# Optimization experiments

Measured on AMD Instinct MI355X. Metric: run time of the kernel, lower is better.

Reference implementation:

```python
import jax, jax.numpy as jnp
import numpy as np
import jax.scipy.linalg

BATCH = 1048576
M_NUM = 2
DT = 0.0166667
NN_RATIO = 0.5
SLOPE = 0.01  # torch LeakyReLU default negative_slope


def setup_inputs() -> dict:
    key = jax.random.key(0)
    ks = jax.random.split(key, 16)
    inp = {}
    inp["SS"] = jax.random.normal(ks[0], (BATCH, 2), dtype=jnp.float32)
    inp["Alphas"] = jax.random.uniform(ks[1], (BATCH, M_NUM), dtype=jnp.float32)
    # per-muscle scalar parameters (positive so sqrt(K*I) is valid)
    inp["K0s"] = jax.random.uniform(ks[2], (M_NUM,), minval=0.5, maxval=1.5)
    inp["K1s"] = jax.random.uniform(ks[3], (M_NUM,), minval=0.5, maxval=1.5)
    inp["L0s"] = jax.random.uniform(ks[4], (M_NUM,), minval=0.5, maxval=1.5)
    inp["L1s"] = jax.random.uniform(ks[5], (M_NUM,), minval=0.1, maxval=0.6)
    inp["Ms"] = jnp.array([1.0, -1.0], dtype=jnp.float32)  # moment arms
    inp["I_p"] = jnp.array([1.0], dtype=jnp.float32)
    inp["B_p"] = jnp.array([0.05], dtype=jnp.float32)
    inp["K_p"] = jnp.array([1.0], dtype=jnp.float32)
    # per-muscle compensational MLP weights: 3-32-32-32-1 (eval mode, dropout off)
    s = 0.1
    inp["W1"] = jax.random.normal(ks[6], (M_NUM, 3, 32)) * s
    inp["b1"] = jax.random.normal(ks[7], (M_NUM, 32)) * s
    inp["W2"] = jax.random.normal(ks[8], (M_NUM, 32, 32)) * s
    inp["b2"] = jax.random.normal(ks[9], (M_NUM, 32)) * s
    inp["W3"] = jax.random.normal(ks[10], (M_NUM, 32, 32)) * s
    inp["b3"] = jax.random.normal(ks[11], (M_NUM, 32)) * s
    inp["W4"] = jax.random.normal(ks[12], (M_NUM, 32, 1)) * s
    inp["b4"] = jax.random.normal(ks[13], (M_NUM, 1)) * s
    return inp


def _leaky(x):
    return jnp.where(x >= 0, x, SLOPE * x)


def reference(SS, Alphas, K0s, K1s, L0s, L1s, Ms, I_p, B_p, K_p,
              W1, b1, W2, b2, W3, b3, W4, b4):
    B = SS.shape[0]
    a = jnp.clip(Alphas, 0.0, 1.0)                      # (B, m)
    # muscle length / speed via scalar moment arms
    l = SS[:, 0:1] * Ms[None, :]                        # (B, m)
    dl = SS[:, 1:2] * Ms[None, :]                       # (B, m)
    # compensational MLPs, vectorized over muscles
    x = jnp.stack([l, dl, a], axis=-1)                  # (B, m, 3)
    h = _leaky(jnp.einsum('bmi,mio->bmo', x, W1) + b1[None])
    h = _leaky(jnp.einsum('bmi,mio->bmo', h, W2) + b2[None])
    h = _leaky(jnp.einsum('bmi,mio->bmo', h, W3) + b3[None])
    nn_out = jnp.tanh(jnp.einsum('bmi,mio->bmo', h, W4) + b4[None])[..., 0] * NN_RATIO  # (B, m)

    I0, B0p, K0p = I_p[0], B_p[0], K_p[0]
    K_m = K0s[None, :] + K1s[None, :] * a               # (B, m)
    K_tot = jnp.sum(K_m * Ms[None, :] ** 2, axis=1)     # (B,)
    A10 = -(K_tot + K0p) / I0
    D = 2.0 * jnp.sqrt(K_tot * I0)
    A11 = -(D + B0p) / I0
    B_F = K_m * (L0s[None, :] + L1s[None, :] * a - jnp.abs(l)) \
        + K1s[None, :] * L1s[None, :] * a * a * nn_out   # (B, m)
    B10 = jnp.sum(B_F * Ms[None, :], axis=1) / I0       # (B,)

    # Build block matrix M6 = [[A*dt, B*dt, 0], [0, 0, I2], [0, 0, 0]]
    M6 = jnp.zeros((B, 6, 6), dtype=SS.dtype)
    M6 = M6.at[:, 0, 1].set(DT)
    M6 = M6.at[:, 1, 0].set(A10 * DT)
    M6 = M6.at[:, 1, 1].set(A11 * DT)
    M6 = M6.at[:, 1, 2].set(B10 * DT)
    M6 = M6.at[:, 1, 3].set(DT / I0)
    M6 = M6.at[:, 2, 4].set(1.0)
    M6 = M6.at[:, 3, 5].set(1.0)

    expMT = jax.vmap(jax.scipy.linalg.expm)(M6)         # (B, 6, 6)
    Ad = expMT[:, :2, :2]
    Bd1 = expMT[:, :2, 4:6]
    Bd0 = expMT[:, :2, 2:4] - Bd1
    u = jnp.array([1.0, 0.0], dtype=SS.dtype)           # U0 = U1 = [1, 0]
    SSout = (jnp.einsum('bij,bj->bi', Ad, SS)
             + jnp.einsum('bij,j->bi', Bd0, u)
             + jnp.einsum('bij,j->bi', Bd1, u))          # (B, 2)
    return SSout[:, :1], SSout
```

## Files before the change

### kernel.cpp

```cpp
#include <hip/hip_runtime.h>
#include <hip/hip_bf16.h>

#define NTHREADS 256
#define WAVES    4
#define GPW      4
#define DT_F     0.0166667f

typedef _Float16 f16x4 __attribute__((ext_vector_type(4)));
typedef _Float16 f16x2 __attribute__((ext_vector_type(2)));
typedef __fp16   hf2   __attribute__((ext_vector_type(2)));
typedef float    f32x4 __attribute__((ext_vector_type(4)));

#define BF16_PROBE 0xBF803F80u

#define OW1 0
#define OB1 192
#define OW2 256
#define OB2 2304
#define OW3 2368
#define OB3 4416
#define OW4 4480
#define OB4 4544
#define SMEM_F 4560

__device__ __forceinline__ float leaky(float x) { return fmaxf(x, 0.01f * x); }

__device__ __forceinline__ float tanh_fast(float x) {
    const float xc = fminf(fmaxf(x, -10.0f), 10.0f);
    const float t  = __expf(2.0f * xc);
    return (t - 1.0f) * __builtin_amdgcn_rcpf(t + 1.0f);
}

__device__ __forceinline__ f16x2 pkrtz(float a, float b) {
    return __builtin_bit_cast(f16x2, __builtin_amdgcn_cvt_pkrtz(a, b));
}

__device__ __forceinline__ f16x4 leaky_cvt(const f32x4 D) {
    f16x2 lo = pkrtz(D[0], D[1]);
    f16x2 hi = pkrtz(D[2], D[3]);
    const f16x2 sl = {(_Float16)0.01f, (_Float16)0.01f};
    lo = __builtin_elementwise_max(lo, lo * sl);
    hi = __builtin_elementwise_max(hi, hi * sl);
    return __builtin_shufflevector(lo, hi, 0, 1, 2, 3);
}

__device__ __forceinline__ void epilogue_math(
    const float* P, float ss0, float ss1, float a0, float a1,
    float nn0, float nn1, float& o0f, float& o1f)
{
    const float K00 = P[0], K01 = P[1], K10 = P[2], K11 = P[3];
    const float L00 = P[4], L01 = P[5], L10 = P[6], L11 = P[7];
    const float Ms0 = P[8], Ms1 = P[9];
    const float I0  = P[10], B0p = P[11], K0p = P[12];

    const float Km0   = fmaf(K10, a0, K00);
    const float Km1   = fmaf(K11, a1, K01);
    const float K_tot = Km0*Ms0*Ms0 + Km1*Ms1*Ms1;
    const float invI  = 1.0f / I0;
    const float A10   = -(K_tot + K0p) * invI;
    const float Dd    = 2.0f * sqrtf(K_tot * I0);
    const float A11   = -(Dd + B0p) * invI;
    const float absl0 = fabsf(ss0 * Ms0);
    const float absl1 = fabsf(ss0 * Ms1);
    const float BF0   = Km0 * (L00 + L10*a0 - absl0) + K10*L10*a0*a0*nn0;
    const float BF1   = Km1 * (L01 + L11*a1 - absl1) + K11*L11*a1*a1*nn1;
    const float B10   = (BF0*Ms0 + BF1*Ms1) * invI;

    const float t01 = DT_F;
    const float t10 = A10 * DT_F;
    const float t11 = A11 * DT_F;

    float p00 = 1.0f/5040.0f, p01 = 0.0f, p10 = 0.0f, p11 = 1.0f/5040.0f;
    const float coef[6] = {1.0f/720.0f, 1.0f/120.0f, 1.0f/24.0f,
                           1.0f/6.0f,   0.5f,        1.0f};
    #pragma unroll
    for (int j = 0; j < 6; ++j) {
        const float cj  = coef[j];
        const float n00 = p01*t10 + cj;
        const float n01 = p00*t01 + p01*t11;
        const float n10 = p11*t10;
        const float n11 = p10*t01 + p11*t11 + cj;
        p00 = n00; p01 = n01; p10 = n10; p11 = n11;
    }
    const float e00 = 1.0f + t01*p10;
    const float e01 = t01*p11;
    const float e10 = t10*p00 + t11*p10;
    const float e11 = 1.0f + t10*p01 + t11*p11;

    const float cscale = DT_F * B10;
    o0f = fmaf(e00, ss0, fmaf(e01, ss1, p01 * cscale));
    o1f = fmaf(e10, ss0, fmaf(e11, ss1, p11 * cscale));
}

__device__ __forceinline__ float ldb(const __hip_bfloat16* p, int i) {
    return __bfloat162float(p[i]);
}

__device__ void run_bf16_fallback(
    const void* SSv, const void* ALv, const void* K0sv, const void* K1sv,
    const void* L0sv, const void* L1sv, const void* Msv, const void* I_pv,
    const void* B_pv, const void* K_pv, const void* W1v, const void* b1v,
    const void* W2v, const void* b2v, const void* W3v, const void* b3v,
    const void* W4v, const void* b4v, void* outv, int batch)
{
    const __hip_bfloat16* SS = (const __hip_bfloat16*)SSv;
    const __hip_bfloat16* AL = (const __hip_bfloat16*)ALv;
    const __hip_bfloat16* W1 = (const __hip_bfloat16*)W1v;
    const __hip_bfloat16* b1 = (const __hip_bfloat16*)b1v;
    const __hip_bfloat16* W2 = (const __hip_bfloat16*)W2v;
    const __hip_bfloat16* b2 = (const __hip_bfloat16*)b2v;
    const __hip_bfloat16* W3 = (const __hip_bfloat16*)W3v;
    const __hip_bfloat16* b3 = (const __hip_bfloat16*)b3v;
    const __hip_bfloat16* W4 = (const __hip_bfloat16*)W4v;
    const __hip_bfloat16* b4 = (const __hip_bfloat16*)b4v;

    float P[13];
    P[0] = ldb((const __hip_bfloat16*)K0sv, 0); P[1] = ldb((const __hip_bfloat16*)K0sv, 1);
    P[2] = ldb((const __hip_bfloat16*)K1sv, 0); P[3] = ldb((const __hip_bfloat16*)K1sv, 1);
    P[4] = ldb((const __hip_bfloat16*)L0sv, 0); P[5] = ldb((const __hip_bfloat16*)L0sv, 1);
    P[6] = ldb((const __hip_bfloat16*)L1sv, 0); P[7] = ldb((const __hip_bfloat16*)L1sv, 1);
    P[8] = ldb((const __hip_bfloat16*)Msv, 0);  P[9] = ldb((const __hip_bfloat16*)Msv, 1);
    P[10] = ldb((const __hip_bfloat16*)I_pv, 0);
    P[11] = ldb((const __hip_bfloat16*)B_pv, 0);
    P[12] = ldb((const __hip_bfloat16*)K_pv, 0);

    const int stride = gridDim.x * blockDim.x;
    for (int e = blockIdx.x * blockDim.x + threadIdx.x; e < batch; e += stride) {
        const float ss0 = ldb(SS, 2*e), ss1 = ldb(SS, 2*e+1);
        float a0 = fminf(fmaxf(ldb(AL, 2*e),   0.0f), 1.0f);
        float a1 = fminf(fmaxf(ldb(AL, 2*e+1), 0.0f), 1.0f);
        float nn[2];
        #pragma unroll 1
        for (int m = 0; m < 2; ++m) {
            const float am = m ? a1 : a0;
            const float l = ss0 * P[8+m], dl = ss1 * P[8+m];
            float h[32];
            #pragma unroll
            for (int o = 0; o < 32; ++o)
                h[o] = leaky(fmaf(l, ldb(W1, m*96+o),
                             fmaf(dl, ldb(W1, m*96+32+o),
                             fmaf(am, ldb(W1, m*96+64+o), ldb(b1, m*32+o)))));
            float g[32];
            #pragma unroll 1
            for (int oc = 0; oc < 4; ++oc) {
                float acc[8];
                #pragma unroll
                for (int j = 0; j < 8; ++j) acc[j] = ldb(b2, m*32+oc*8+j);
                #pragma unroll
                for (int k = 0; k < 32; ++k) {
                    #pragma unroll
                    for (int j = 0; j < 8; ++j)
                        acc[j] = fmaf(h[k], ldb(W2, m*1024+k*32+oc*8+j), acc[j]);
                }
                #pragma unroll
                for (int j = 0; j < 8; ++j) g[oc*8+j] = leaky(acc[j]);
            }
            float h3[32];
            #pragma unroll 1
            for (int oc = 0; oc < 4; ++oc) {
                float acc[8];
                #pragma unroll
                for (int j = 0; j < 8; ++j) acc[j] = ldb(b3, m*32+oc*8+j);
                #pragma unroll
                for (int k = 0; k < 32; ++k) {
                    #pragma unroll
                    for (int j = 0; j < 8; ++j)
                        acc[j] = fmaf(g[k], ldb(W3, m*1024+k*32+oc*8+j), acc[j]);
                }
                #pragma unroll
                for (int j = 0; j < 8; ++j) h3[oc*8+j] = leaky(acc[j]);
            }
            float acc = ldb(b4, m);
            #pragma unroll
            for (int k = 0; k < 32; ++k) acc = fmaf(h3[k], ldb(W4, m*32+k), acc);
            nn[m] = tanh_fast(acc) * 0.5f;
        }
        float o0f, o1f;
        epilogue_math(P, ss0, ss1, a0, a1, nn[0], nn[1], o0f, o1f);
        __hip_bfloat16* out0 = (__hip_bfloat16*)outv;
        __hip_bfloat162* out1 = (__hip_bfloat162*)(out0 + batch);
        out0[e] = __float2bfloat16(o0f);
        __hip_bfloat162 pr;
        pr.x = __float2bfloat16(o0f);
        pr.y = __float2bfloat16(o1f);
        out1[e] = pr;
    }
}

__global__ __launch_bounds__(NTHREADS) void joint_kernel(
    const void* __restrict__ SSv, const void* __restrict__ ALv,
    const void* __restrict__ K0sv, const void* __restrict__ K1sv,
    const void* __restrict__ L0sv, const void* __restrict__ L1sv,
    const void* __restrict__ Msv,  const void* __restrict__ I_pv,
    const void* __restrict__ B_pv, const void* __restrict__ K_pv,
    const void* __restrict__ W1v,  const void* __restrict__ b1v,
    const void* __restrict__ W2v,  const void* __restrict__ b2v,
    const void* __restrict__ W3v,  const void* __restrict__ b3v,
    const void* __restrict__ W4v,  const void* __restrict__ b4v,
    void* __restrict__ outv, int batch)
{
    const unsigned probe = *(const unsigned*)Msv;
    if (probe == BF16_PROBE) {
        run_bf16_fallback(SSv, ALv, K0sv, K1sv, L0sv, L1sv, Msv, I_pv, B_pv,
                          K_pv, W1v, b1v, W2v, b2v, W3v, b3v, W4v, b4v,
                          outv, batch);
        return;
    }

    const float* SS = (const float*)SSv;
    const float* AL = (const float*)ALv;
    const float* W1 = (const float*)W1v;  const float* b1 = (const float*)b1v;
    const float* W2 = (const float*)W2v;  const float* b2 = (const float*)b2v;
    const float* W3 = (const float*)W3v;  const float* b3 = (const float*)b3v;
    const float* W4 = (const float*)W4v;  const float* b4 = (const float*)b4v;

    const int tid  = threadIdx.x;
    const int wave = tid >> 6;
    const int lane = tid & 63;
    const int n    = lane & 15;
    const int q    = lane >> 4;

    __shared__ __align__(16) float sm[SMEM_F];
    for (int i = tid; i < 192;  i += NTHREADS) sm[OW1+i] = W1[i];
    for (int i = tid; i < 2048; i += NTHREADS) { sm[OW2+i] = W2[i]; sm[OW3+i] = W3[i]; }
    for (int i = tid; i < 64;   i += NTHREADS) {
        sm[OB1+i] = b1[i]; sm[OB2+i] = b2[i];
        sm[OB3+i] = b3[i]; sm[OW4+i] = W4[i];
    }
    if (tid < 2) sm[OB4+tid] = b4[tid];
    __syncthreads();

    f16x4 A1[2][2];
    #pragma unroll
    for (int mi = 0; mi < 2; ++mi)
        #pragma unroll
        for (int i = 0; i < 2; ++i)
            #pragma unroll
            for (int j = 0; j < 4; ++j) {
                const int k = q*4 + j;
                float v = 0.0f;
                if (k < 3)       v = sm[OW1 + mi*96 + k*32 + i*16 + n];
                else if (k == 3) v = sm[OB1 + mi*32 + i*16 + n];
                A1[mi][i][j] = (_Float16)v;
            }
    f16x4 A2[2][2][2], A3[2][2][2];
    #pragma unroll
    for (int mi = 0; mi < 2; ++mi)
        #pragma unroll
        for (int i = 0; i < 2; ++i)
            #pragma unroll
            for (int kb = 0; kb < 2; ++kb)
                #pragma unroll
                for (int j = 0; j < 4; ++j) {
                    const int in = kb*16 + q*4 + j;
                    A2[mi][i][kb][j] = (_Float16)sm[OW2 + mi*1024 + in*32 + i*16 + n];
                    A3[mi][i][kb][j] = (_Float16)sm[OW3 + mi*1024 + in*32 + i*16 + n];
                }
    f16x4 A4[2][2];
    #pragma unroll
    for (int mi = 0; mi < 2; ++mi)
        #pragma unroll
        for (int kb = 0; kb < 2; ++kb)
            #pragma unroll
            for (int j = 0; j < 4; ++j)
                A4[mi][kb][j] = (_Float16)sm[OW4 + mi*32 + kb*16 + q*4 + j];
    f32x4 Cb2[2][2], Cb3[2][2];
    #pragma unroll
    for (int mi = 0; mi < 2; ++mi)
        #pragma unroll
        for (int i = 0; i < 2; ++i) {
            Cb2[mi][i] = *(const f32x4*)&sm[OB2 + mi*32 + i*16 + q*4];
            Cb3[mi][i] = *(const f32x4*)&sm[OB3 + mi*32 + i*16 + q*4];
        }
    const float b4s0 = sm[OB4], b4s1 = sm[OB4+1];

    float P[13];
    P[0]  = ((const float*)K0sv)[0]; P[1]  = ((const float*)K0sv)[1];
    P[2]  = ((const float*)K1sv)[0]; P[3]  = ((const float*)K1sv)[1];
    P[4]  = ((const float*)L0sv)[0]; P[5]  = ((const float*)L0sv)[1];
    P[6]  = ((const float*)L1sv)[0]; P[7]  = ((const float*)L1sv)[1];
    P[8]  = ((const float*)Msv)[0];  P[9]  = ((const float*)Msv)[1];
    P[10] = ((const float*)I_pv)[0];
    P[11] = ((const float*)B_pv)[0];
    P[12] = ((const float*)K_pv)[0];

    const f32x4 zero = {0.0f, 0.0f, 0.0f, 0.0f};
    const bool q0 = (q == 0);
    const int groupBase = (blockIdx.x * WAVES + wave) * GPW;

    #pragma unroll 1
    for (int g = 0; g < GPW; ++g) {
        const int ebase = (groupBase + g) * 64;
        float my_sx = 0.0f, my_sy = 0.0f, my_a0 = 0.0f, my_a1 = 0.0f;
        float my_r0 = 0.0f, my_r1 = 0.0f;

        #pragma unroll
        for (int t = 0; t < 4; ++t) {
            const int e  = ebase + t*16 + n;
            const int eg = min(e, batch - 1);
            const float2 s  = ((const float2*)SS)[eg];
            const float2 al = ((const float2*)AL)[eg];
            const float a0 = fminf(fmaxf(al.x, 0.0f), 1.0f);
            const float a1 = fminf(fmaxf(al.y, 0.0f), 1.0f);

            float rr[2];
            #pragma unroll
            for (int mi = 0; mi < 2; ++mi) {
                const float Msm = P[8 + mi];
                const float am  = mi ? a1 : a0;
                const f16x2 blo = pkrtz(q0 ? s.x * Msm : 0.0f,
                                        q0 ? s.y * Msm : 0.0f);
                const f16x2 bhi = pkrtz(q0 ? am : 0.0f, q0 ? 1.0f : 0.0f);
                const f16x4 B1 = __builtin_shufflevector(blo, bhi, 0, 1, 2, 3);

                f32x4 D0 = __builtin_amdgcn_mfma_f32_16x16x16f16(A1[mi][0], B1, zero, 0, 0, 0);
                f32x4 D1 = __builtin_amdgcn_mfma_f32_16x16x16f16(A1[mi][1], B1, zero, 0, 0, 0);
                const f16x4 B2_0 = leaky_cvt(D0);
                const f16x4 B2_1 = leaky_cvt(D1);

                f32x4 E0 = __builtin_amdgcn_mfma_f32_16x16x16f16(A2[mi][0][1], B2_1,
                           __builtin_amdgcn_mfma_f32_16x16x16f16(A2[mi][0][0], B2_0,
                               Cb2[mi][0], 0, 0, 0), 0, 0, 0);
                f32x4 E1 = __builtin_amdgcn_mfma_f32_16x16x16f16(A2[mi][1][1], B2_1,
                           __builtin_amdgcn_mfma_f32_16x16x16f16(A2[mi][1][0], B2_0,
                               Cb2[mi][1], 0, 0, 0), 0, 0, 0);
                const f16x4 B3_0 = leaky_cvt(E0);
                const f16x4 B3_1 = leaky_cvt(E1);

                f32x4 F0 = __builtin_amdgcn_mfma_f32_16x16x16f16(A3[mi][0][1], B3_1,
                           __builtin_amdgcn_mfma_f32_16x16x16f16(A3[mi][0][0], B3_0,
                               Cb3[mi][0], 0, 0, 0), 0, 0, 0);
                f32x4 F1 = __builtin_amdgcn_mfma_f32_16x16x16f16(A3[mi][1][1], B3_1,
                           __builtin_amdgcn_mfma_f32_16x16x16f16(A3[mi][1][0], B3_0,
                               Cb3[mi][1], 0, 0, 0), 0, 0, 0);
                const f16x4 B4_0 = leaky_cvt(F0);
                const f16x4 B4_1 = leaky_cvt(F1);

                f32x4 G = __builtin_amdgcn_mfma_f32_16x16x16f16(A4[mi][1], B4_1,
                          __builtin_amdgcn_mfma_f32_16x16x16f16(A4[mi][0], B4_0,
                              zero, 0, 0, 0), 0, 0, 0);
                rr[mi] = G[0] + (mi ? b4s1 : b4s0);
            }

            const bool own = (q == t);
            my_sx = own ? s.x : my_sx;
            my_sy = own ? s.y : my_sy;
            my_a0 = own ? a0  : my_a0;
            my_a1 = own ? a1  : my_a1;
            my_r0 = own ? rr[0] : my_r0;
            my_r1 = own ? rr[1] : my_r1;
        }

        const int eo = ebase + lane;
        const float nn0 = tanh_fast(my_r0) * 0.5f;
        const float nn1 = tanh_fast(my_r1) * 0.5f;
        float o0f, o1f;
        epilogue_math(P, my_sx, my_sy, my_a0, my_a1, nn0, nn1, o0f, o1f);
        if (eo < batch) {
            ((float*)outv)[eo] = o0f;
            ((float2*)((float*)outv + batch))[eo] = make_float2(o0f, o1f);
        }
    }
}

extern "C" void kernel_launch(void* const* d_in, const int* in_sizes, int n_in,
                              void* d_out, int out_size, void* d_ws, size_t ws_size,
                              hipStream_t stream) {
    const int batch = in_sizes[0] / 2;
    const int elemsPerBlock = 64 * GPW * WAVES;
    const int grid = (batch + elemsPerBlock - 1) / elemsPerBlock;
    joint_kernel<<<grid, NTHREADS, 0, stream>>>(
        d_in[0], d_in[1], d_in[2], d_in[3], d_in[4], d_in[5], d_in[6],
        d_in[7], d_in[8], d_in[9], d_in[10], d_in[11], d_in[12], d_in[13],
        d_in[14], d_in[15], d_in[16], d_in[17], d_out, batch);
}
```

Measured before the change: 132.5 us.

## Shrink per-wave work, raise occupancy, fold output bias into MFMA, reload inputs

Halves the groups processed per wave and adds a minimum-blocks hint of 6 to launch_bounds, so the compiler holds fewer registers and more waves fit per CU. The final-layer bias now goes in as the MFMA accumulator initializer rather than a separate add. The q==0 masking on the first-layer B operand is dropped. Each lane now reloads its own SS and Alphas row for the epilogue instead of carrying select-tracked copies through the t loop. This saves VGPRs and selects, but adds a second global read of the inputs and launches more blocks. Dropping the mask relies on the A1 layout zeroing the unused k rows.

```diff
diff --git a/kernel.cpp b/kernel.cpp
--- a/kernel.cpp
+++ b/kernel.cpp
@@ -3,12 +3,11 @@
 
 #define NTHREADS 256
 #define WAVES    4
-#define GPW      4
+#define GPW      2
 #define DT_F     0.0166667f
 
 typedef _Float16 f16x4 __attribute__((ext_vector_type(4)));
 typedef _Float16 f16x2 __attribute__((ext_vector_type(2)));
-typedef __fp16   hf2   __attribute__((ext_vector_type(2)));
 typedef float    f32x4 __attribute__((ext_vector_type(4)));
 
 #define BF16_PROBE 0xBF803F80u
@@ -187,7 +186,7 @@
     }
 }
 
-__global__ __launch_bounds__(NTHREADS) void joint_kernel(
+__global__ __launch_bounds__(NTHREADS, 6) void joint_kernel(
     const void* __restrict__ SSv, const void* __restrict__ ALv,
     const void* __restrict__ K0sv, const void* __restrict__ K1sv,
     const void* __restrict__ L0sv, const void* __restrict__ L1sv,
@@ -264,15 +263,17 @@
             #pragma unroll
             for (int j = 0; j < 4; ++j)
                 A4[mi][kb][j] = (_Float16)sm[OW4 + mi*32 + kb*16 + q*4 + j];
-    f32x4 Cb2[2][2], Cb3[2][2];
-    #pragma unroll
-    for (int mi = 0; mi < 2; ++mi)
+    f32x4 Cb2[2][2], Cb3[2][2], Cb4[2];
+    #pragma unroll
+    for (int mi = 0; mi < 2; ++mi) {
         #pragma unroll
         for (int i = 0; i < 2; ++i) {
             Cb2[mi][i] = *(const f32x4*)&sm[OB2 + mi*32 + i*16 + q*4];
             Cb3[mi][i] = *(const f32x4*)&sm[OB3 + mi*32 + i*16 + q*4];
         }
-    const float b4s0 = sm[OB4], b4s1 = sm[OB4+1];
+        const float b4s = sm[OB4 + mi];
+        Cb4[mi] = (f32x4){b4s, b4s, b4s, b4s};
+    }
 
     float P[13];
     P[0]  = ((const float*)K0sv)[0]; P[1]  = ((const float*)K0sv)[1];
@@ -285,13 +286,11 @@
     P[12] = ((const float*)K_pv)[0];
 
     const f32x4 zero = {0.0f, 0.0f, 0.0f, 0.0f};
-    const bool q0 = (q == 0);
     const int groupBase = (blockIdx.x * WAVES + wave) * GPW;
 
     #pragma unroll 1
     for (int g = 0; g < GPW; ++g) {
         const int ebase = (groupBase + g) * 64;
-        float my_sx = 0.0f, my_sy = 0.0f, my_a0 = 0.0f, my_a1 = 0.0f;
         float my_r0 = 0.0f, my_r1 = 0.0f;
 
         #pragma unroll
@@ -308,9 +307,8 @@
             for (int mi = 0; mi < 2; ++mi) {
                 const float Msm = P[8 + mi];
                 const float am  = mi ? a1 : a0;
-                const f16x2 blo = pkrtz(q0 ? s.x * Msm : 0.0f,
-                                        q0 ? s.y * Msm : 0.0f);
-                const f16x2 bhi = pkrtz(q0 ? am : 0.0f, q0 ? 1.0f : 0.0f);
+                const f16x2 blo = pkrtz(s.x * Msm, s.y * Msm);
+                const f16x2 bhi = pkrtz(am, 1.0f);
                 const f16x4 B1 = __builtin_shufflevector(blo, bhi, 0, 1, 2, 3);
 
                 f32x4 D0 = __builtin_amdgcn_mfma_f32_16x16x16f16(A1[mi][0], B1, zero, 0, 0, 0);
@@ -338,24 +336,25 @@
 
                 f32x4 G = __builtin_amdgcn_mfma_f32_16x16x16f16(A4[mi][1], B4_1,
                           __builtin_amdgcn_mfma_f32_16x16x16f16(A4[mi][0], B4_0,
-                              zero, 0, 0, 0), 0, 0, 0);
-                rr[mi] = G[0] + (mi ? b4s1 : b4s0);
+                              Cb4[mi], 0, 0, 0), 0, 0, 0);
+                rr[mi] = G[0];
             }
 
             const bool own = (q == t);
-            my_sx = own ? s.x : my_sx;
-            my_sy = own ? s.y : my_sy;
-            my_a0 = own ? a0  : my_a0;
-            my_a1 = own ? a1  : my_a1;
             my_r0 = own ? rr[0] : my_r0;
             my_r1 = own ? rr[1] : my_r1;
         }
 
-        const int eo = ebase + lane;
+        const int eo  = ebase + lane;
+        const int eog = min(eo, batch - 1);
+        const float2 s  = ((const float2*)SS)[eog];
+        const float2 al = ((const float2*)AL)[eog];
+        const float a0 = fminf(fmaxf(al.x, 0.0f), 1.0f);
+        const float a1 = fminf(fmaxf(al.y, 0.0f), 1.0f);
         const float nn0 = tanh_fast(my_r0) * 0.5f;
         const float nn1 = tanh_fast(my_r1) * 0.5f;
         float o0f, o1f;
-        epilogue_math(P, my_sx, my_sy, my_a0, my_a1, nn0, nn1, o0f, o1f);
+        epilogue_math(P, s.x, s.y, a0, a1, nn0, nn1, o0f, o1f);
         if (eo < batch) {
             ((float*)outv)[eo] = o0f;
             ((float2*)((float*)outv + batch))[eo] = make_float2(o0f, o1f);
```

Result: slower. 337.2 us (+154.5%).
